# Performance work log

Measured on AMD Instinct MI355X. Metric: run time of the kernel, lower is better.

Reference implementation:

```python
import jax, jax.numpy as jnp
import numpy as np

N = 50000
E = 400000
IN_DIM = 128
HID = 128
OUT = 128
HEADS = 4
NEG_SLOPE = 0.2
EPS = 1e-16


def setup_inputs() -> dict:
    key = jax.random.key(0)
    ks = jax.random.split(key, 12)
    s = 0.05
    return {
        "x": jax.random.normal(ks[0], (N, IN_DIM), dtype=jnp.float32),
        "edge_index": jax.random.randint(ks[1], (2, E), 0, N, dtype=jnp.int64),
        # layer 1: in_dim -> hid, heads=4, concat
        "W1": jax.random.normal(ks[2], (IN_DIM, HEADS * HID), dtype=jnp.float32) * s,
        "att_src1": jax.random.normal(ks[3], (HEADS, HID), dtype=jnp.float32) * s,
        "att_dst1": jax.random.normal(ks[4], (HEADS, HID), dtype=jnp.float32) * s,
        "bias1": jnp.zeros((HEADS * HID,), dtype=jnp.float32),
        # layer 2: hid*heads -> out, heads=1, no concat
        "W2": jax.random.normal(ks[5], (HEADS * HID, OUT), dtype=jnp.float32) * s,
        "att_src2": jax.random.normal(ks[6], (1, OUT), dtype=jnp.float32) * s,
        "att_dst2": jax.random.normal(ks[7], (1, OUT), dtype=jnp.float32) * s,
        "bias2": jnp.zeros((OUT,), dtype=jnp.float32),
    }


def gat_conv(x, src, dst, W, att_src, att_dst, bias, heads, out_dim, concat):
    n = x.shape[0]
    h = (x @ W).reshape(n, heads, out_dim)                       # [N,H,D]
    a_src = jnp.sum(h * att_src[None], axis=-1)                  # [N,H]
    a_dst = jnp.sum(h * att_dst[None], axis=-1)                  # [N,H]
    e = jax.nn.leaky_relu(a_src[src] + a_dst[dst], NEG_SLOPE)    # [E,H]
    # segment softmax over incoming edges of each dst node
    e_max = jax.ops.segment_max(e, dst, num_segments=n)          # [N,H]
    ex = jnp.exp(e - e_max[dst])
    denom = jax.ops.segment_sum(ex, dst, num_segments=n)         # [N,H]
    alpha = ex / (denom[dst] + EPS)                              # [E,H]
    msg = h[src] * alpha[..., None]                              # [E,H,D]
    out = jax.ops.segment_sum(msg, dst, num_segments=n)          # [N,H,D]
    out = out.reshape(n, heads * out_dim) if concat else out.mean(axis=1)
    return out + bias


def reference(x, edge_index, W1, att_src1, att_dst1, bias1, W2, att_src2, att_dst2, bias2):
    n = x.shape[0]
    loop = jnp.arange(n, dtype=edge_index.dtype)
    src = jnp.concatenate([edge_index[0], loop])  # PyG add_self_loops=True
    dst = jnp.concatenate([edge_index[1], loop])
    h = jax.nn.elu(gat_conv(x, src, dst, W1, att_src1, att_dst1, bias1, HEADS, HID, True))
    z = jax.nn.elu(gat_conv(h, src, dst, W2, att_src2, att_dst2, bias2, 1, OUT, False))
    # F.normalize(z, dim=-1): L2 with eps=1e-12 clamp on the norm
    norm = jnp.maximum(jnp.linalg.norm(z, axis=-1, keepdims=True), 1e-12)
    return z / norm
```

## Files before the change

kernel.cpp:

```cpp
#include <hip/hip_runtime.h>
#include <cstddef>

#define N_NODES 50000
#define N_EDGES 400000
#define TOT_EDGES (N_EDGES + N_NODES)
#define M_PAD 50048
#define SCAN_PAD 50176
#define NBLK 49
#define CNT_BLKS 1758

typedef _Float16 f16;
typedef __attribute__((ext_vector_type(8))) _Float16 f16x8;
typedef __attribute__((ext_vector_type(4))) _Float16 f16x4;
typedef __attribute__((ext_vector_type(2))) _Float16 f16x2;
typedef __attribute__((ext_vector_type(4))) float f32x4;

__device__ __forceinline__ float lrelu(float e) { return e > 0.f ? e : 0.2f * e; }

__global__ void zero_int(int* __restrict__ p, int n) {
  int i = blockIdx.x * blockDim.x + threadIdx.x;
  if (i < n) p[i] = 0;
}

__global__ __launch_bounds__(256) void count_weights(
    const int* __restrict__ ei, int* __restrict__ deg,
    const float* __restrict__ W1, const float* __restrict__ W2,
    const float* __restrict__ att_s1, const float* __restrict__ att_d1,
    const float* __restrict__ att_s2, const float* __restrict__ att_d2,
    f16* __restrict__ w1t, f16* __restrict__ w2t,
    float* __restrict__ V1s, float* __restrict__ V1d,
    float* __restrict__ V2s, float* __restrict__ V2d) {
  const int b = blockIdx.x;
  if (b < CNT_BLKS) {
    const int e = b * 256 + threadIdx.x;
    if (e >= TOT_EDGES) return;
    const int dst = (e < N_EDGES) ? ei[N_EDGES + e] : (e - N_EDGES);
    atomicAdd(&deg[dst], 1);
    return;
  }
  const int bb = b - CNT_BLKS;
  if (bb < 256) {
    const int idx = bb * 256 + threadIdx.x;
    const int cc = idx >> 7, rr = idx & 127;
    w1t[idx] = (f16)W1[(size_t)rr * 512 + cc];
  } else if (bb < 512) {
    const int idx = (bb - 256) * 256 + threadIdx.x;
    const int cc = idx >> 9, rr = idx & 511;
    w2t[idx] = (f16)W2[(size_t)rr * 128 + cc];
  } else if (bb < 640) {
    const int wid = (bb - 512) * 4 + (threadIdx.x >> 6);
    const int lane = threadIdx.x & 63;
    const int k = wid >> 2, h = wid & 3;
    const float* wrow = W1 + (size_t)k * 512 + h * 128;
    float2 wv = *(const float2*)&wrow[lane * 2];
    float2 sv = *(const float2*)&att_s1[h * 128 + lane * 2];
    float2 dv = *(const float2*)&att_d1[h * 128 + lane * 2];
    float ps = wv.x * sv.x + wv.y * sv.y;
    float pd = wv.x * dv.x + wv.y * dv.y;
#pragma unroll
    for (int off = 32; off; off >>= 1) {
      ps += __shfl_xor(ps, off);
      pd += __shfl_xor(pd, off);
    }
    if (lane == 0) { V1s[k * 4 + h] = ps; V1d[k * 4 + h] = pd; }
  } else {
    const int wid = (bb - 640) * 4 + (threadIdx.x >> 6);
    const int lane = threadIdx.x & 63;
    const float* wrow = W2 + (size_t)wid * 128;
    float2 wv = *(const float2*)&wrow[lane * 2];
    float2 sv = *(const float2*)&att_s2[lane * 2];
    float2 dv = *(const float2*)&att_d2[lane * 2];
    float ps = wv.x * sv.x + wv.y * sv.y;
    float pd = wv.x * dv.x + wv.y * dv.y;
#pragma unroll
    for (int off = 32; off; off >>= 1) {
      ps += __shfl_xor(ps, off);
      pd += __shfl_xor(pd, off);
    }
    if (lane == 0) { V2s[wid] = ps; V2d[wid] = pd; }
  }
}

__global__ __launch_bounds__(256) void histscan_prepx(
    const int* __restrict__ deg, int* __restrict__ pre, int* __restrict__ bsum,
    int* __restrict__ blkcnt,
    const float* __restrict__ x, f16* __restrict__ xb,
    const float* __restrict__ V1s, const float* __restrict__ V1d,
    float* __restrict__ as1, float* __restrict__ ad1, f16* __restrict__ aggb) {
  __shared__ int wsum[4];
  __shared__ int lh[128];
  const int b = blockIdx.x;
  if (b < NBLK) {
    const int t = threadIdx.x, lane = t & 63, w = t >> 6;
    if (t < 128) lh[t] = 0;
    __syncthreads();
    const int base = b * 1024 + t * 4;
    int4 v = *(const int4*)&deg[base];
    if (base + 0 < N_NODES) atomicAdd(&lh[min(v.x, 127)], 1);
    if (base + 1 < N_NODES) atomicAdd(&lh[min(v.y, 127)], 1);
    if (base + 2 < N_NODES) atomicAdd(&lh[min(v.z, 127)], 1);
    if (base + 3 < N_NODES) atomicAdd(&lh[min(v.w, 127)], 1);
    const int s = v.x + v.y + v.z + v.w;
    int xx = s;
#pragma unroll
    for (int off = 1; off < 64; off <<= 1) {
      int y = __shfl_up(xx, off);
      if (lane >= off) xx += y;
    }
    if (lane == 63) wsum[w] = xx;
    __syncthreads();
    int woff = 0;
    for (int j = 0; j < w; ++j) woff += wsum[j];
    const int ex = xx - s + woff;
    pre[base + 0] = ex;
    pre[base + 1] = ex + v.x;
    pre[base + 2] = ex + v.x + v.y;
    pre[base + 3] = ex + v.x + v.y + v.z;
    if (t == 255) bsum[b] = ex + s;
    if (t < 128) blkcnt[t * NBLK + b] = lh[t];
    return;
  }
  const int wid = (b - NBLK) * 4 + (threadIdx.x >> 6);
  const int lane = threadIdx.x & 63;
  const int k = lane * 2;
  if (wid >= N_NODES) {
    f16x2 z; z[0] = (f16)0.f; z[1] = (f16)0.f;
    *(f16x2*)&xb[(size_t)wid * 128 + k] = z;
    f16x8 z8;
#pragma unroll
    for (int j = 0; j < 8; ++j) z8[j] = (f16)0.f;
    *(f16x8*)&aggb[(size_t)wid * 512 + lane * 8] = z8;
    return;
  }
  float2 xv = *(const float2*)&x[(size_t)wid * 128 + k];
  f16x2 o; o[0] = (f16)xv.x; o[1] = (f16)xv.y;
  *(f16x2*)&xb[(size_t)wid * 128 + k] = o;
  float4 vs0 = *(const float4*)&V1s[k * 4];
  float4 vs1 = *(const float4*)&V1s[(k + 1) * 4];
  float4 vd0 = *(const float4*)&V1d[k * 4];
  float4 vd1 = *(const float4*)&V1d[(k + 1) * 4];
  float s[4], d[4];
  s[0] = xv.x * vs0.x + xv.y * vs1.x;
  s[1] = xv.x * vs0.y + xv.y * vs1.y;
  s[2] = xv.x * vs0.z + xv.y * vs1.z;
  s[3] = xv.x * vs0.w + xv.y * vs1.w;
  d[0] = xv.x * vd0.x + xv.y * vd1.x;
  d[1] = xv.x * vd0.y + xv.y * vd1.y;
  d[2] = xv.x * vd0.z + xv.y * vd1.z;
  d[3] = xv.x * vd0.w + xv.y * vd1.w;
#pragma unroll
  for (int h = 0; h < 4; ++h) {
#pragma unroll
    for (int off = 32; off; off >>= 1) {
      s[h] += __shfl_xor(s[h], off);
      d[h] += __shfl_xor(d[h], off);
    }
  }
  if (lane == 0) {
    *(float4*)&as1[(size_t)wid * 4] = make_float4(s[0], s[1], s[2], s[3]);
    *(float4*)&ad1[(size_t)wid * 4] = make_float4(d[0], d[1], d[2], d[3]);
  }
}

__global__ __launch_bounds__(128) void scan2(int* __restrict__ bsum,
                                             const int* __restrict__ blkcnt,
                                             int* __restrict__ boff) {
  __shared__ int tot[128];
  const int t = threadIdx.x;
  int s = 0;
  for (int k = 0; k < NBLK; ++k) s += blkcnt[t * NBLK + k];
  tot[t] = s;
  __syncthreads();
  if (t == 0) {
    int acc = 0;
    for (int b = 0; b < 128; ++b) { const int v = tot[b]; tot[b] = acc; acc += v; }
  }
  __syncthreads();
  int acc = tot[t];
  for (int k = 0; k < NBLK; ++k) {
    boff[t * NBLK + k] = acc;
    acc += blkcnt[t * NBLK + k];
  }
  if (t < 64) {
    int v = (t < NBLK) ? bsum[t] : 0;
    int xx = v;
#pragma unroll
    for (int off = 1; off < 64; off <<= 1) {
      int y = __shfl_up(xx, off);
      if (t >= off) xx += y;
    }
    if (t < NBLK) bsum[t] = xx - v;
  }
}

__global__ __launch_bounds__(256) void scatter_addoff(
    int* __restrict__ pre, const int* __restrict__ bsumoff,
    int* __restrict__ cursor, const int* __restrict__ deg,
    const int* __restrict__ boff, int* __restrict__ order) {
  __shared__ int lcur[128];
  const int t = threadIdx.x;
  const int b = blockIdx.x;
  if (t < 128) lcur[t] = boff[t * NBLK + b];
  __syncthreads();
  const int base4 = b * 1024 + t * 4;
  const int off = bsumoff[b];
  int4 v = *(const int4*)&pre[base4];
  v.x += off; v.y += off; v.z += off; v.w += off;
  *(int4*)&pre[base4] = v;
  *(int4*)&cursor[base4] = v;
#pragma unroll
  for (int j = 0; j < 4; ++j) {
    const int i = b * 1024 + j * 256 + t;
    if (i < N_NODES) {
      const int bk = min(deg[i], 127);
      const int pos = atomicAdd(&lcur[bk], 1);
      order[pos] = i;
    }
  }
}

__global__ void fill_w1(const int* __restrict__ ei, int* __restrict__ cursor,
                        const float* __restrict__ as1, const float* __restrict__ ad1,
                        int* __restrict__ csr, int* __restrict__ csrd,
                        float* __restrict__ wexp1) {
  const int e = blockIdx.x * blockDim.x + threadIdx.x;
  if (e >= TOT_EDGES) return;
  int s, d;
  if (e < N_EDGES) { s = ei[e]; d = ei[N_EDGES + e]; }
  else             { s = d = e - N_EDGES; }
  const int pos = atomicAdd(&cursor[d], 1);
  csr[pos] = s;
  csrd[pos] = d;
  float4 a = *(const float4*)&as1[(size_t)s * 4];
  float4 bz = *(const float4*)&ad1[(size_t)d * 4];
  float4 w;
  w.x = __expf(lrelu(a.x + bz.x));
  w.y = __expf(lrelu(a.y + bz.y));
  w.z = __expf(lrelu(a.z + bz.z));
  w.w = __expf(lrelu(a.w + bz.w));
  *(float4*)&wexp1[(size_t)pos * 4] = w;
}

__global__ void edge_w2(const int* __restrict__ csr, const int* __restrict__ csrd,
                        const float* __restrict__ as2, const float* __restrict__ ad2,
                        float* __restrict__ w2exp) {
  const int kk = blockIdx.x * blockDim.x + threadIdx.x;
  if (kk >= TOT_EDGES) return;
  w2exp[kk] = __expf(lrelu(as2[csr[kk]] + ad2[csrd[kk]]));
}

template <int K, bool PER_HEAD, bool FUSE_A2>
__global__ __launch_bounds__(256) void gemm_bt(const f16* __restrict__ A, int lda,
                                               const f16* __restrict__ Bt, int ldb,
                                               f16* __restrict__ C, int ldc,
                                               const float* __restrict__ bias,
                                               const float* __restrict__ V2s,
                                               const float* __restrict__ V2d,
                                               float* __restrict__ as2,
                                               float* __restrict__ ad2) {
  if constexpr (PER_HEAD) {
    const int hh = blockIdx.y;
    A += (size_t)hh * 128;
    Bt += (size_t)hh * 128 * 128;
    C += (size_t)hh * 128;
    bias += hh * 128;
  }
  constexpr int LDT = 40;
  __shared__ __align__(16) f16 As[128 * LDT];
  __shared__ __align__(16) f16 Bs[128 * LDT];
  const int tid = threadIdx.x;
  const int lane = tid & 63;
  const int g = lane >> 4, r16 = lane & 15;
  const int w = tid >> 6, wr = w >> 1, wc = w & 1;
  const long bm = (long)blockIdx.x * 128;

  const int row0 = tid >> 2, h0 = tid & 3;
  const int p1 = (h0 & 1) * 16 + (h0 >> 1) * 4;
  const size_t ga0 = (size_t)(bm + row0) * lda + h0 * 8;
  const size_t ga1 = (size_t)(bm + row0 + 64) * lda + h0 * 8;
  const size_t gb0 = (size_t)row0 * ldb + h0 * 8;
  const size_t gb1 = (size_t)(row0 + 64) * ldb + h0 * 8;
  const int la0 = row0 * LDT + p1, la1 = (row0 + 64) * LDT + p1;

  f32x4 acc[4][4] = {};
  float s2a = 0.f, d2a = 0.f, s2b = 0.f, d2b = 0.f;

  for (int k0 = 0; k0 < K; k0 += 32) {
    __syncthreads();
    f16x8 va0 = *(const f16x8*)&A[ga0 + k0];
    f16x8 va1 = *(const f16x8*)&A[ga1 + k0];
    f16x8 vb0 = *(const f16x8*)&Bt[gb0 + k0];
    f16x8 vb1 = *(const f16x8*)&Bt[gb1 + k0];
    if constexpr (FUSE_A2) {
      const int kc = k0 + h0 * 8;
      float4 vsa = *(const float4*)&V2s[kc];
      float4 vsb = *(const float4*)&V2s[kc + 4];
      float4 vda = *(const float4*)&V2d[kc];
      float4 vdb = *(const float4*)&V2d[kc + 4];
      const float vs[8] = {vsa.x, vsa.y, vsa.z, vsa.w, vsb.x, vsb.y, vsb.z, vsb.w};
      const float vd[8] = {vda.x, vda.y, vda.z, vda.w, vdb.x, vdb.y, vdb.z, vdb.w};
#pragma unroll
      for (int j = 0; j < 8; ++j) {
        s2a += (float)va0[j] * vs[j];
        d2a += (float)va0[j] * vd[j];
        s2b += (float)va1[j] * vs[j];
        d2b += (float)va1[j] * vd[j];
      }
    }
    *(f16x4*)&As[la0]     = __builtin_shufflevector(va0, va0, 0, 1, 2, 3);
    *(f16x4*)&As[la0 + 8] = __builtin_shufflevector(va0, va0, 4, 5, 6, 7);
    *(f16x4*)&As[la1]     = __builtin_shufflevector(va1, va1, 0, 1, 2, 3);
    *(f16x4*)&As[la1 + 8] = __builtin_shufflevector(va1, va1, 4, 5, 6, 7);
    *(f16x4*)&Bs[la0]     = __builtin_shufflevector(vb0, vb0, 0, 1, 2, 3);
    *(f16x4*)&Bs[la0 + 8] = __builtin_shufflevector(vb0, vb0, 4, 5, 6, 7);
    *(f16x4*)&Bs[la1]     = __builtin_shufflevector(vb1, vb1, 0, 1, 2, 3);
    *(f16x4*)&Bs[la1 + 8] = __builtin_shufflevector(vb1, vb1, 4, 5, 6, 7);
    __syncthreads();
    f16x8 af[4], bfv[4];
#pragma unroll
    for (int m = 0; m < 4; ++m)
      af[m] = *(const f16x8*)&As[(wr * 64 + m * 16 + r16) * LDT + g * 8];
#pragma unroll
    for (int n = 0; n < 4; ++n)
      bfv[n] = *(const f16x8*)&Bs[(wc * 64 + n * 16 + r16) * LDT + g * 8];
#pragma unroll
    for (int m = 0; m < 4; ++m)
#pragma unroll
      for (int n = 0; n < 4; ++n)
        acc[m][n] = __builtin_amdgcn_mfma_f32_16x16x32_f16(af[m], bfv[n], acc[m][n], 0, 0, 0);
  }

  if constexpr (FUSE_A2) {
    s2a += __shfl_xor(s2a, 1); s2a += __shfl_xor(s2a, 2);
    d2a += __shfl_xor(d2a, 1); d2a += __shfl_xor(d2a, 2);
    s2b += __shfl_xor(s2b, 1); s2b += __shfl_xor(s2b, 2);
    d2b += __shfl_xor(d2b, 1); d2b += __shfl_xor(d2b, 2);
    if ((tid & 3) == 0) {
      const long r0 = bm + row0;
      as2[r0] = s2a; ad2[r0] = d2a;
      as2[r0 + 64] = s2b; ad2[r0 + 64] = d2b;
    }
  }

#pragma unroll
  for (int m = 0; m < 4; ++m) {
#pragma unroll
    for (int n = 0; n < 4; ++n) {
      const long row = bm + wr * 64 + m * 16 + g * 4;
      const int col = wc * 64 + n * 16 + r16;
      float bv = 0.f;
      if constexpr (PER_HEAD) bv = bias[col];
#pragma unroll
      for (int r = 0; r < 4; ++r) {
        float v = acc[m][n][r];
        if constexpr (PER_HEAD) {
          v += bv;
          v = v > 0.f ? v : (__expf(v) - 1.f);
        }
        C[(size_t)(row + r) * ldc + col] = (f16)v;
      }
    }
  }
}

__global__ __launch_bounds__(256) void aggregate1x(
    const f16* __restrict__ xsrc, const float* __restrict__ wexp,
    const int* __restrict__ rowstart, const int* __restrict__ csr,
    const int* __restrict__ order, f16* __restrict__ aggb) {
  const int wave = (blockIdx.x * blockDim.x + threadIdx.x) >> 6;
  const int lane = threadIdx.x & 63;
  const int g16 = lane >> 4, l16 = lane & 15;
  const int node = order[wave * 4 + g16];
  const int col0 = l16 * 8;
  const int rs = rowstart[node];
  const int re = rowstart[node + 1];
  const int deg = re - rs;

  int maxdeg = deg;
  maxdeg = max(maxdeg, __shfl_xor(maxdeg, 16));
  maxdeg = max(maxdeg, __shfl_xor(maxdeg, 32));

  constexpr int D = 4;
  int sreg[D];
  float4 wreg[D];
  f16x8 hreg[D];
#pragma unroll
  for (int p = 0; p < D; ++p) {
    const int k = rs + p;
    const int kc = (k < re) ? k : (re - 1);
    wreg[p] = *(const float4*)&wexp[(size_t)kc * 4];
    const int s = csr[kc];
    hreg[p] = *(const f16x8*)&xsrc[(size_t)s * 128 + col0];
    const int k2 = rs + D + p;
    sreg[p] = csr[(k2 < re) ? k2 : (re - 1)];
  }

  float acc0[8] = {}, acc1[8] = {}, acc2[8] = {}, acc3[8] = {};
  float Z0 = 0.f, Z1 = 0.f, Z2 = 0.f, Z3 = 0.f;
  for (int base = 0; base < maxdeg; base += D) {
#pragma unroll
    for (int p = 0; p < D; ++p) {
      const int i = base + p;
      const bool act = i < deg;
      float4 wv = wreg[p];
      const float w0 = act ? wv.x : 0.f;
      const float w1 = act ? wv.y : 0.f;
      const float w2 = act ? wv.z : 0.f;
      const float w3 = act ? wv.w : 0.f;
      const f16x8 h = hreg[p];
      const int nk = rs + i + D;
      if (nk < re) {
        wreg[p] = *(const float4*)&wexp[(size_t)nk * 4];
        const int s = sreg[p];
        hreg[p] = *(const f16x8*)&xsrc[(size_t)s * 128 + col0];
      }
      const int nk2 = rs + i + 2 * D;
      if (nk2 < re) sreg[p] = csr[nk2];
      Z0 += w0; Z1 += w1; Z2 += w2; Z3 += w3;
#pragma unroll
      for (int j = 0; j < 8; ++j) {
        const float hv = (float)h[j];
        acc0[j] += w0 * hv;
        acc1[j] += w1 * hv;
        acc2[j] += w2 * hv;
        acc3[j] += w3 * hv;
      }
    }
  }

  const float i0 = 1.f / (Z0 + 1e-16f);
  const float i1 = 1.f / (Z1 + 1e-16f);
  const float i2 = 1.f / (Z2 + 1e-16f);
  const float i3 = 1.f / (Z3 + 1e-16f);
  f16* orow = aggb + (size_t)node * 512 + col0;
  f16x8 o0, o1, o2, o3;
#pragma unroll
  for (int j = 0; j < 8; ++j) {
    o0[j] = (f16)(acc0[j] * i0);
    o1[j] = (f16)(acc1[j] * i1);
    o2[j] = (f16)(acc2[j] * i2);
    o3[j] = (f16)(acc3[j] * i3);
  }
  *(f16x8*)&orow[0]   = o0;
  *(f16x8*)&orow[128] = o1;
  *(f16x8*)&orow[256] = o2;
  *(f16x8*)&orow[384] = o3;
}

__global__ __launch_bounds__(256) void aggregate2(
    const f16* __restrict__ hsrc, const float* __restrict__ w2exp,
    const int* __restrict__ rowstart, const int* __restrict__ csr,
    const int* __restrict__ order, const float* __restrict__ bias,
    float* __restrict__ out) {
  const int wave = (blockIdx.x * blockDim.x + threadIdx.x) >> 6;
  const int lane = threadIdx.x & 63;
  const int g16 = lane >> 4, l16 = lane & 15;
  const int node = order[wave * 4 + g16];
  const int col0 = l16 * 8;
  const int rs = rowstart[node];
  const int re = rowstart[node + 1];
  const int deg = re - rs;

  int maxdeg = deg;
  maxdeg = max(maxdeg, __shfl_xor(maxdeg, 16));
  maxdeg = max(maxdeg, __shfl_xor(maxdeg, 32));

  constexpr int D = 6;
  int sreg[D];
  float wreg[D];
  f16x8 hreg[D];
#pragma unroll
  for (int p = 0; p < D; ++p) {
    const int k = rs + p;
    const int kc = (k < re) ? k : (re - 1);
    wreg[p] = w2exp[kc];
    const int s = csr[kc];
    hreg[p] = *(const f16x8*)&hsrc[(size_t)s * 128 + col0];
    const int k2 = rs + D + p;
    sreg[p] = csr[(k2 < re) ? k2 : (re - 1)];
  }

  float acc[8] = {};
  float Z = 0.f;
  for (int base = 0; base < maxdeg; base += D) {
#pragma unroll
    for (int p = 0; p < D; ++p) {
      const int i = base + p;
      const bool act = i < deg;
      const float w = act ? wreg[p] : 0.f;
      const f16x8 h = hreg[p];
      const int nk = rs + i + D;
      if (nk < re) {
        wreg[p] = w2exp[nk];
        const int s = sreg[p];
        hreg[p] = *(const f16x8*)&hsrc[(size_t)s * 128 + col0];
      }
      const int nk2 = rs + i + 2 * D;
      if (nk2 < re) sreg[p] = csr[nk2];
      Z += w;
#pragma unroll
      for (int j = 0; j < 8; ++j) acc[j] += w * (float)h[j];
    }
  }
  const float inv = 1.f / (Z + 1e-16f);

  float4 ba = *(const float4*)&bias[col0];
  float4 bb = *(const float4*)&bias[col0 + 4];
  const float bv[8] = {ba.x, ba.y, ba.z, ba.w, bb.x, bb.y, bb.z, bb.w};
  float v[8];
  float ss = 0.f;
#pragma unroll
  for (int j = 0; j < 8; ++j) {
    float t = acc[j] * inv + bv[j];
    t = t > 0.f ? t : (__expf(t) - 1.f);
    v[j] = t;
    ss += t * t;
  }
  ss += __shfl_xor(ss, 1);
  ss += __shfl_xor(ss, 2);
  ss += __shfl_xor(ss, 4);
  ss += __shfl_xor(ss, 8);
  const float invn = 1.f / fmaxf(sqrtf(ss), 1e-12f);
  float* orow = out + (size_t)node * 128 + col0;
  float4 oa = make_float4(v[0] * invn, v[1] * invn, v[2] * invn, v[3] * invn);
  float4 ob = make_float4(v[4] * invn, v[5] * invn, v[6] * invn, v[7] * invn);
  *(float4*)&orow[0] = oa;
  *(float4*)&orow[4] = ob;
}

extern "C" void kernel_launch(void* const* d_in, const int* in_sizes, int n_in,
                              void* d_out, int out_size, void* d_ws, size_t ws_size,
                              hipStream_t stream) {
  const float* x        = (const float*)d_in[0];
  const int*   ei       = (const int*)d_in[1];
  const float* W1       = (const float*)d_in[2];
  const float* att_src1 = (const float*)d_in[3];
  const float* att_dst1 = (const float*)d_in[4];
  const float* bias1    = (const float*)d_in[5];
  const float* W2       = (const float*)d_in[6];
  const float* att_src2 = (const float*)d_in[7];
  const float* att_dst2 = (const float*)d_in[8];
  const float* bias2    = (const float*)d_in[9];
  float* out = (float*)d_out;

  char* ws = (char*)d_ws;
  size_t off = 0;
  auto alloc = [&](size_t bytes) {
    char* p = ws + off;
    off = (off + bytes + 255) & ~(size_t)255;
    return p;
  };
  f16* xb    = (f16*)alloc(sizeof(f16) * (size_t)M_PAD * 128);
  f16* w1t   = (f16*)alloc(sizeof(f16) * 512 * 128);
  f16* w2t   = (f16*)alloc(sizeof(f16) * 128 * 512);
  f16* aggb  = (f16*)alloc(sizeof(f16) * (size_t)M_PAD * 512);
  f16* out1b = (f16*)alloc(sizeof(f16) * (size_t)M_PAD * 512);
  float* V1s = (float*)alloc(sizeof(float) * 512);
  float* V1d = (float*)alloc(sizeof(float) * 512);
  float* V2s = (float*)alloc(sizeof(float) * 512);
  float* V2d = (float*)alloc(sizeof(float) * 512);
  float* as1 = (float*)alloc(sizeof(float) * N_NODES * 4);
  float* ad1 = (float*)alloc(sizeof(float) * N_NODES * 4);
  float* as2 = (float*)alloc(sizeof(float) * M_PAD);
  float* ad2 = (float*)alloc(sizeof(float) * M_PAD);
  float* wexp1 = (float*)alloc(sizeof(float) * (size_t)TOT_EDGES * 4);
  float* w2exp = (float*)alloc(sizeof(float) * TOT_EDGES);
  int* rowstart = (int*)alloc(sizeof(int) * (SCAN_PAD + 4));
  int* deg      = (int*)alloc(sizeof(int) * SCAN_PAD);
  int* cursor   = (int*)alloc(sizeof(int) * SCAN_PAD);
  int* bsum     = (int*)alloc(sizeof(int) * 64);
  int* blkcnt   = (int*)alloc(sizeof(int) * 128 * NBLK);
  int* boff     = (int*)alloc(sizeof(int) * 128 * NBLK);
  int* order    = (int*)alloc(sizeof(int) * N_NODES);
  int* csr      = (int*)alloc(sizeof(int) * TOT_EDGES);
  int* csrd     = (int*)alloc(sizeof(int) * TOT_EDGES);
  f16* h2b = aggb;

  const int agrid = (N_NODES / 4) * 64 / 256;

  zero_int<<<(SCAN_PAD + 255) / 256, 256, 0, stream>>>(deg, SCAN_PAD);
  count_weights<<<CNT_BLKS + 768, 256, 0, stream>>>(
      ei, deg, W1, W2, att_src1, att_dst1, att_src2, att_dst2,
      w1t, w2t, V1s, V1d, V2s, V2d);
  histscan_prepx<<<NBLK + M_PAD / 4, 256, 0, stream>>>(
      deg, rowstart, bsum, blkcnt, x, xb, V1s, V1d, as1, ad1, aggb);
  scan2<<<1, 128, 0, stream>>>(bsum, blkcnt, boff);
  scatter_addoff<<<NBLK, 256, 0, stream>>>(rowstart, bsum, cursor, deg, boff, order);
  fill_w1<<<CNT_BLKS, 256, 0, stream>>>(ei, cursor, as1, ad1, csr, csrd, wexp1);
  aggregate1x<<<agrid, 256, 0, stream>>>(xb, wexp1, rowstart, csr, order, aggb);
  gemm_bt<128, true, false><<<dim3(M_PAD / 128, 4), 256, 0, stream>>>(
      aggb, 512, w1t, 128, out1b, 512, bias1, nullptr, nullptr, nullptr, nullptr);
  gemm_bt<512, false, true><<<dim3(M_PAD / 128, 1), 256, 0, stream>>>(
      out1b, 512, w2t, 512, h2b, 128, nullptr, V2s, V2d, as2, ad2);
  edge_w2<<<CNT_BLKS, 256, 0, stream>>>(csr, csrd, as2, ad2, w2exp);
  aggregate2<<<agrid, 256, 0, stream>>>(h2b, w2exp, rowstart, csr, order, bias2, out);
}
```

Measured before the change: 199.7 us.

## Fuse layer-2 edge weights into aggregation, deepen GEMM K tile, reorder aggregation nodes

```diff
diff --git a/kernel.cpp b/kernel.cpp
--- a/kernel.cpp
+++ b/kernel.cpp
@@ -221,8 +221,7 @@
 
 __global__ void fill_w1(const int* __restrict__ ei, int* __restrict__ cursor,
                         const float* __restrict__ as1, const float* __restrict__ ad1,
-                        int* __restrict__ csr, int* __restrict__ csrd,
-                        float* __restrict__ wexp1) {
+                        int* __restrict__ csr, float* __restrict__ wexp1) {
   const int e = blockIdx.x * blockDim.x + threadIdx.x;
   if (e >= TOT_EDGES) return;
   int s, d;
@@ -230,7 +229,6 @@
   else             { s = d = e - N_EDGES; }
   const int pos = atomicAdd(&cursor[d], 1);
   csr[pos] = s;
-  csrd[pos] = d;
   float4 a = *(const float4*)&as1[(size_t)s * 4];
   float4 bz = *(const float4*)&ad1[(size_t)d * 4];
   float4 w;
@@ -239,14 +237,6 @@
   w.z = __expf(lrelu(a.z + bz.z));
   w.w = __expf(lrelu(a.w + bz.w));
   *(float4*)&wexp1[(size_t)pos * 4] = w;
-}
-
-__global__ void edge_w2(const int* __restrict__ csr, const int* __restrict__ csrd,
-                        const float* __restrict__ as2, const float* __restrict__ ad2,
-                        float* __restrict__ w2exp) {
-  const int kk = blockIdx.x * blockDim.x + threadIdx.x;
-  if (kk >= TOT_EDGES) return;
-  w2exp[kk] = __expf(lrelu(as2[csr[kk]] + ad2[csrd[kk]]));
 }
 
 template <int K, bool PER_HEAD, bool FUSE_A2>
@@ -265,7 +255,7 @@
     C += (size_t)hh * 128;
     bias += hh * 128;
   }
-  constexpr int LDT = 40;
+  constexpr int LDT = 72;
   __shared__ __align__(16) f16 As[128 * LDT];
   __shared__ __align__(16) f16 Bs[128 * LDT];
   const int tid = threadIdx.x;
@@ -285,49 +275,69 @@
   f32x4 acc[4][4] = {};
   float s2a = 0.f, d2a = 0.f, s2b = 0.f, d2b = 0.f;
 
-  for (int k0 = 0; k0 < K; k0 += 32) {
+  for (int k0 = 0; k0 < K; k0 += 64) {
     __syncthreads();
-    f16x8 va0 = *(const f16x8*)&A[ga0 + k0];
-    f16x8 va1 = *(const f16x8*)&A[ga1 + k0];
-    f16x8 vb0 = *(const f16x8*)&Bt[gb0 + k0];
-    f16x8 vb1 = *(const f16x8*)&Bt[gb1 + k0];
+    f16x8 a0k0 = *(const f16x8*)&A[ga0 + k0];
+    f16x8 a0k1 = *(const f16x8*)&A[ga0 + k0 + 32];
+    f16x8 a1k0 = *(const f16x8*)&A[ga1 + k0];
+    f16x8 a1k1 = *(const f16x8*)&A[ga1 + k0 + 32];
+    f16x8 b0k0 = *(const f16x8*)&Bt[gb0 + k0];
+    f16x8 b0k1 = *(const f16x8*)&Bt[gb0 + k0 + 32];
+    f16x8 b1k0 = *(const f16x8*)&Bt[gb1 + k0];
+    f16x8 b1k1 = *(const f16x8*)&Bt[gb1 + k0 + 32];
     if constexpr (FUSE_A2) {
-      const int kc = k0 + h0 * 8;
-      float4 vsa = *(const float4*)&V2s[kc];
-      float4 vsb = *(const float4*)&V2s[kc + 4];
-      float4 vda = *(const float4*)&V2d[kc];
-      float4 vdb = *(const float4*)&V2d[kc + 4];
-      const float vs[8] = {vsa.x, vsa.y, vsa.z, vsa.w, vsb.x, vsb.y, vsb.z, vsb.w};
-      const float vd[8] = {vda.x, vda.y, vda.z, vda.w, vdb.x, vdb.y, vdb.z, vdb.w};
-#pragma unroll
-      for (int j = 0; j < 8; ++j) {
-        s2a += (float)va0[j] * vs[j];
-        d2a += (float)va0[j] * vd[j];
-        s2b += (float)va1[j] * vs[j];
-        d2b += (float)va1[j] * vd[j];
-      }
-    }
-    *(f16x4*)&As[la0]     = __builtin_shufflevector(va0, va0, 0, 1, 2, 3);
-    *(f16x4*)&As[la0 + 8] = __builtin_shufflevector(va0, va0, 4, 5, 6, 7);
-    *(f16x4*)&As[la1]     = __builtin_shufflevector(va1, va1, 0, 1, 2, 3);
-    *(f16x4*)&As[la1 + 8] = __builtin_shufflevector(va1, va1, 4, 5, 6, 7);
-    *(f16x4*)&Bs[la0]     = __builtin_shufflevector(vb0, vb0, 0, 1, 2, 3);
-    *(f16x4*)&Bs[la0 + 8] = __builtin_shufflevector(vb0, vb0, 4, 5, 6, 7);
-    *(f16x4*)&Bs[la1]     = __builtin_shufflevector(vb1, vb1, 0, 1, 2, 3);
-    *(f16x4*)&Bs[la1 + 8] = __builtin_shufflevector(vb1, vb1, 4, 5, 6, 7);
+#pragma unroll
+      for (int c = 0; c < 2; ++c) {
+        const int kc = k0 + c * 32 + h0 * 8;
+        const f16x8 va = c ? a0k1 : a0k0;
+        const f16x8 vb = c ? a1k1 : a1k0;
+        float4 vsa = *(const float4*)&V2s[kc];
+        float4 vsb = *(const float4*)&V2s[kc + 4];
+        float4 vda = *(const float4*)&V2d[kc];
+        float4 vdb = *(const float4*)&V2d[kc + 4];
+        const float vs[8] = {vsa.x, vsa.y, vsa.z, vsa.w, vsb.x, vsb.y, vsb.z, vsb.w};
+        const float vd[8] = {vda.x, vda.y, vda.z, vda.w, vdb.x, vdb.y, vdb.z, vdb.w};
+#pragma unroll
+        for (int j = 0; j < 8; ++j) {
+          s2a += (float)va[j] * vs[j];
+          d2a += (float)va[j] * vd[j];
+          s2b += (float)vb[j] * vs[j];
+          d2b += (float)vb[j] * vd[j];
+        }
+      }
+    }
+    *(f16x4*)&As[la0]      = __builtin_shufflevector(a0k0, a0k0, 0, 1, 2, 3);
+    *(f16x4*)&As[la0 + 8]  = __builtin_shufflevector(a0k0, a0k0, 4, 5, 6, 7);
+    *(f16x4*)&As[la0 + 32] = __builtin_shufflevector(a0k1, a0k1, 0, 1, 2, 3);
+    *(f16x4*)&As[la0 + 40] = __builtin_shufflevector(a0k1, a0k1, 4, 5, 6, 7);
+    *(f16x4*)&As[la1]      = __builtin_shufflevector(a1k0, a1k0, 0, 1, 2, 3);
+    *(f16x4*)&As[la1 + 8]  = __builtin_shufflevector(a1k0, a1k0, 4, 5, 6, 7);
+    *(f16x4*)&As[la1 + 32] = __builtin_shufflevector(a1k1, a1k1, 0, 1, 2, 3);
+    *(f16x4*)&As[la1 + 40] = __builtin_shufflevector(a1k1, a1k1, 4, 5, 6, 7);
+    *(f16x4*)&Bs[la0]      = __builtin_shufflevector(b0k0, b0k0, 0, 1, 2, 3);
+    *(f16x4*)&Bs[la0 + 8]  = __builtin_shufflevector(b0k0, b0k0, 4, 5, 6, 7);
+    *(f16x4*)&Bs[la0 + 32] = __builtin_shufflevector(b0k1, b0k1, 0, 1, 2, 3);
+    *(f16x4*)&Bs[la0 + 40] = __builtin_shufflevector(b0k1, b0k1, 4, 5, 6, 7);
+    *(f16x4*)&Bs[la1]      = __builtin_shufflevector(b1k0, b1k0, 0, 1, 2, 3);
+    *(f16x4*)&Bs[la1 + 8]  = __builtin_shufflevector(b1k0, b1k0, 4, 5, 6, 7);
+    *(f16x4*)&Bs[la1 + 32] = __builtin_shufflevector(b1k1, b1k1, 0, 1, 2, 3);
+    *(f16x4*)&Bs[la1 + 40] = __builtin_shufflevector(b1k1, b1k1, 4, 5, 6, 7);
     __syncthreads();
-    f16x8 af[4], bfv[4];
-#pragma unroll
-    for (int m = 0; m < 4; ++m)
-      af[m] = *(const f16x8*)&As[(wr * 64 + m * 16 + r16) * LDT + g * 8];
-#pragma unroll
-    for (int n = 0; n < 4; ++n)
-      bfv[n] = *(const f16x8*)&Bs[(wc * 64 + n * 16 + r16) * LDT + g * 8];
-#pragma unroll
-    for (int m = 0; m < 4; ++m)
+#pragma unroll
+    for (int ks = 0; ks < 2; ++ks) {
+      f16x8 af[4], bfv[4];
+#pragma unroll
+      for (int m = 0; m < 4; ++m)
+        af[m] = *(const f16x8*)&As[(wr * 64 + m * 16 + r16) * LDT + ks * 32 + g * 8];
 #pragma unroll
       for (int n = 0; n < 4; ++n)
-        acc[m][n] = __builtin_amdgcn_mfma_f32_16x16x32_f16(af[m], bfv[n], acc[m][n], 0, 0, 0);
+        bfv[n] = *(const f16x8*)&Bs[(wc * 64 + n * 16 + r16) * LDT + ks * 32 + g * 8];
+#pragma unroll
+      for (int m = 0; m < 4; ++m)
+#pragma unroll
+        for (int n = 0; n < 4; ++n)
+          acc[m][n] = __builtin_amdgcn_mfma_f32_16x16x32_f16(af[m], bfv[n], acc[m][n], 0, 0, 0);
+    }
   }
 
   if constexpr (FUSE_A2) {
@@ -370,15 +380,17 @@
   const int wave = (blockIdx.x * blockDim.x + threadIdx.x) >> 6;
   const int lane = threadIdx.x & 63;
   const int g16 = lane >> 4, l16 = lane & 15;
-  const int node = order[wave * 4 + g16];
+  const int node = order[N_NODES - 1 - (wave * 4 + g16)];
   const int col0 = l16 * 8;
   const int rs = rowstart[node];
   const int re = rowstart[node + 1];
   const int deg = re - rs;
 
-  int maxdeg = deg;
+  int maxdeg = deg, mindeg = deg;
   maxdeg = max(maxdeg, __shfl_xor(maxdeg, 16));
   maxdeg = max(maxdeg, __shfl_xor(maxdeg, 32));
+  mindeg = min(mindeg, __shfl_xor(mindeg, 16));
+  mindeg = min(mindeg, __shfl_xor(mindeg, 32));
 
   constexpr int D = 4;
   int sreg[D];
@@ -397,12 +409,39 @@
 
   float acc0[8] = {}, acc1[8] = {}, acc2[8] = {}, acc3[8] = {};
   float Z0 = 0.f, Z1 = 0.f, Z2 = 0.f, Z3 = 0.f;
-  for (int base = 0; base < maxdeg; base += D) {
+
+  int base = 0;
+  for (; base + D <= mindeg; base += D) {
+#pragma unroll
+    for (int p = 0; p < D; ++p) {
+      const int i = base + p;
+      const float4 wv = wreg[p];
+      const f16x8 h = hreg[p];
+      const int nk = rs + i + D;
+      if (nk < re) {
+        wreg[p] = *(const float4*)&wexp[(size_t)nk * 4];
+        const int s = sreg[p];
+        hreg[p] = *(const f16x8*)&xsrc[(size_t)s * 128 + col0];
+      }
+      const int nk2 = rs + i + 2 * D;
+      if (nk2 < re) sreg[p] = csr[nk2];
+      Z0 += wv.x; Z1 += wv.y; Z2 += wv.z; Z3 += wv.w;
+#pragma unroll
+      for (int j = 0; j < 8; ++j) {
+        const float hv = (float)h[j];
+        acc0[j] += wv.x * hv;
+        acc1[j] += wv.y * hv;
+        acc2[j] += wv.z * hv;
+        acc3[j] += wv.w * hv;
+      }
+    }
+  }
+  for (; base < maxdeg; base += D) {
 #pragma unroll
     for (int p = 0; p < D; ++p) {
       const int i = base + p;
       const bool act = i < deg;
-      float4 wv = wreg[p];
+      const float4 wv = wreg[p];
       const float w0 = act ? wv.x : 0.f;
       const float w1 = act ? wv.y : 0.f;
       const float w2 = act ? wv.z : 0.f;
@@ -448,33 +487,36 @@
 }
 
 __global__ __launch_bounds__(256) void aggregate2(
-    const f16* __restrict__ hsrc, const float* __restrict__ w2exp,
-    const int* __restrict__ rowstart, const int* __restrict__ csr,
-    const int* __restrict__ order, const float* __restrict__ bias,
-    float* __restrict__ out) {
+    const f16* __restrict__ hsrc, const float* __restrict__ as2,
+    const float* __restrict__ ad2, const int* __restrict__ rowstart,
+    const int* __restrict__ csr, const int* __restrict__ order,
+    const float* __restrict__ bias, float* __restrict__ out) {
   const int wave = (blockIdx.x * blockDim.x + threadIdx.x) >> 6;
   const int lane = threadIdx.x & 63;
   const int g16 = lane >> 4, l16 = lane & 15;
-  const int node = order[wave * 4 + g16];
+  const int node = order[N_NODES - 1 - (wave * 4 + g16)];
   const int col0 = l16 * 8;
   const int rs = rowstart[node];
   const int re = rowstart[node + 1];
   const int deg = re - rs;
-
-  int maxdeg = deg;
+  const float ad = ad2[node];
+
+  int maxdeg = deg, mindeg = deg;
   maxdeg = max(maxdeg, __shfl_xor(maxdeg, 16));
   maxdeg = max(maxdeg, __shfl_xor(maxdeg, 32));
+  mindeg = min(mindeg, __shfl_xor(mindeg, 16));
+  mindeg = min(mindeg, __shfl_xor(mindeg, 32));
 
   constexpr int D = 6;
   int sreg[D];
-  float wreg[D];
+  float areg[D];
   f16x8 hreg[D];
 #pragma unroll
   for (int p = 0; p < D; ++p) {
     const int k = rs + p;
     const int kc = (k < re) ? k : (re - 1);
-    wreg[p] = w2exp[kc];
     const int s = csr[kc];
+    areg[p] = as2[s];
     hreg[p] = *(const f16x8*)&hsrc[(size_t)s * 128 + col0];
     const int k2 = rs + D + p;
     sreg[p] = csr[(k2 < re) ? k2 : (re - 1)];
@@ -482,17 +524,37 @@
 
   float acc[8] = {};
   float Z = 0.f;
-  for (int base = 0; base < maxdeg; base += D) {
+  int base = 0;
+  for (; base + D <= mindeg; base += D) {
+#pragma unroll
+    for (int p = 0; p < D; ++p) {
+      const int i = base + p;
+      const float w = __expf(lrelu(areg[p] + ad));
+      const f16x8 h = hreg[p];
+      const int nk = rs + i + D;
+      if (nk < re) {
+        const int s = sreg[p];
+        areg[p] = as2[s];
+        hreg[p] = *(const f16x8*)&hsrc[(size_t)s * 128 + col0];
+      }
+      const int nk2 = rs + i + 2 * D;
+      if (nk2 < re) sreg[p] = csr[nk2];
+      Z += w;
+#pragma unroll
+      for (int j = 0; j < 8; ++j) acc[j] += w * (float)h[j];
+    }
+  }
+  for (; base < maxdeg; base += D) {
 #pragma unroll
     for (int p = 0; p < D; ++p) {
       const int i = base + p;
       const bool act = i < deg;
-      const float w = act ? wreg[p] : 0.f;
+      const float w = act ? __expf(lrelu(areg[p] + ad)) : 0.f;
       const f16x8 h = hreg[p];
       const int nk = rs + i + D;
       if (nk < re) {
-        wreg[p] = w2exp[nk];
         const int s = sreg[p];
+        areg[p] = as2[s];
         hreg[p] = *(const f16x8*)&hsrc[(size_t)s * 128 + col0];
       }
       const int nk2 = rs + i + 2 * D;
@@ -564,7 +626,6 @@
   float* as2 = (float*)alloc(sizeof(float) * M_PAD);
   float* ad2 = (float*)alloc(sizeof(float) * M_PAD);
   float* wexp1 = (float*)alloc(sizeof(float) * (size_t)TOT_EDGES * 4);
-  float* w2exp = (float*)alloc(sizeof(float) * TOT_EDGES);
   int* rowstart = (int*)alloc(sizeof(int) * (SCAN_PAD + 4));
   int* deg      = (int*)alloc(sizeof(int) * SCAN_PAD);
   int* cursor   = (int*)alloc(sizeof(int) * SCAN_PAD);
@@ -573,7 +634,6 @@
   int* boff     = (int*)alloc(sizeof(int) * 128 * NBLK);
   int* order    = (int*)alloc(sizeof(int) * N_NODES);
   int* csr      = (int*)alloc(sizeof(int) * TOT_EDGES);
-  int* csrd     = (int*)alloc(sizeof(int) * TOT_EDGES);
   f16* h2b = aggb;
 
   const int agrid = (N_NODES / 4) * 64 / 256;
@@ -586,12 +646,11 @@
       deg, rowstart, bsum, blkcnt, x, xb, V1s, V1d, as1, ad1, aggb);
   scan2<<<1, 128, 0, stream>>>(bsum, blkcnt, boff);
   scatter_addoff<<<NBLK, 256, 0, stream>>>(rowstart, bsum, cursor, deg, boff, order);
-  fill_w1<<<CNT_BLKS, 256, 0, stream>>>(ei, cursor, as1, ad1, csr, csrd, wexp1);
+  fill_w1<<<CNT_BLKS, 256, 0, stream>>>(ei, cursor, as1, ad1, csr, wexp1);
   aggregate1x<<<agrid, 256, 0, stream>>>(xb, wexp1, rowstart, csr, order, aggb);
   gemm_bt<128, true, false><<<dim3(M_PAD / 128, 4), 256, 0, stream>>>(
       aggb, 512, w1t, 128, out1b, 512, bias1, nullptr, nullptr, nullptr, nullptr);
   gemm_bt<512, false, true><<<dim3(M_PAD / 128, 1), 256, 0, stream>>>(
       out1b, 512, w2t, 512, h2b, 128, nullptr, V2s, V2d, as2, ad2);
-  edge_w2<<<CNT_BLKS, 256, 0, stream>>>(csr, csrd, as2, ad2, w2exp);
-  aggregate2<<<agrid, 256, 0, stream>>>(h2b, w2exp, rowstart, csr, order, bias2, out);
-}
+  aggregate2<<<agrid, 256, 0, stream>>>(h2b, as2, ad2, rowstart, csr, order, bias2, out);
+}
```

After: 192.1 us. 1.04x faster.
